# Kernel tuning notes

Measured on AMD Instinct MI355X. Metric: run time of the kernel, lower is better.

## Reference

```python
import jax, jax.numpy as jnp
import numpy as np

V, E, H, L, S, B = 32000, 1024, 512, 2, 512, 32  # vocab, emb dim, per-dir hidden, layers, seq, batch
PAD = 0
assert E == 2 * H  # required by the module's pred_emb shape assert; lets cell weights stack


def setup_inputs() -> dict:
    ks = iter(jax.random.split(jax.random.key(0), 40))
    def nrm(shape, scale=0.05):
        return jax.random.normal(next(ks), shape, dtype=jnp.float32) * scale
    seq_input = jax.random.randint(next(ks), (S, B), 1, V)
    # lengths sorted descending (pack_padded convention the torch code assumes)
    lengths = jnp.sort(jax.random.randint(next(ks), (B,), S // 2, S + 1))[::-1]
    inp = {"seq_input": seq_input, "lengths": lengths}
    for name in ("emb1", "emb2", "emb3"):
        inp[name] = nrm((V, E)).at[PAD].set(0.0)  # padding_idx row is zero
    inp["W_et"] = nrm((H, E)); inp["b_et"] = nrm((H,))      # embedding_transform
    inp["W_ct"] = nrm((H, H)); inp["b_ct"] = nrm((H,))      # context_transform
    inp["W_sc"] = nrm((1, H)); inp["b_sc"] = nrm((1,))      # to_scalar
    inp["W_g"] = nrm((E, 2 * E)); inp["b_g"] = nrm((E,))    # embedding_gate Linear
    inp["h0f"] = jax.random.uniform(next(ks), (H,), jnp.float32)  # torch.rand init params
    inp["c0f"] = jax.random.uniform(next(ks), (H,), jnp.float32)
    inp["h0b"] = jax.random.uniform(next(ks), (H,), jnp.float32)
    inp["c0b"] = jax.random.uniform(next(ks), (H,), jnp.float32)
    # LSTMCell weights: [layer, dir(fwd,bwd), 4H, in]; in==E==2H for all layers
    inp["Wih"] = nrm((L, 2, 4 * H, E))
    inp["Whh"] = nrm((L, 2, 4 * H, H))
    inp["bih"] = nrm((L, 2, 4 * H))
    inp["bhh"] = nrm((L, 2, 4 * H))
    return inp


def _lstm_cell(x, h, c, Wih, Whh, bih, bhh):
    g = x @ Wih.T + h @ Whh.T + bih + bhh
    i, f, gg, o = jnp.split(g, 4, axis=-1)
    c2 = jax.nn.sigmoid(f) * c + jax.nn.sigmoid(i) * jnp.tanh(gg)
    return jax.nn.sigmoid(o) * jnp.tanh(c2), c2


def _reverse_seq(x, lengths):
    # reverse the first `length` timesteps per batch element, keep padding in place
    t = jnp.arange(x.shape[0])[:, None]
    idx = jnp.where(t < lengths[None, :], lengths[None, :] - 1 - t, t)  # [S,B]
    idx = idx.reshape(idx.shape + (1,) * (x.ndim - 2))
    return jnp.take_along_axis(x, jnp.broadcast_to(idx, x.shape), axis=0)


def _cos(a, b):
    n = jnp.sum(a * b, -1)
    d = jnp.maximum(jnp.linalg.norm(a, axis=-1) * jnp.linalg.norm(b, axis=-1), 1e-8)
    return n / d


def _forward(seq_input, lengths, emb1, emb2, emb3, W_et, b_et, W_ct, b_ct, W_sc, b_sc,
             W_g, b_g, h0f, c0f, h0b, c0b, Wih, Whh, bih, bhh):
    Sl, Bn = seq_input.shape
    Hh = Whh.shape[-1]
    nL = Wih.shape[0]
    # active mask at step t: lengths >= t+1 (identical for forward and reversed scans)
    mask = jnp.arange(Sl)[:, None] < lengths[None, :]  # [S,B]
    h0f_b = jnp.broadcast_to(h0f, (Bn, Hh)); c0f_b = jnp.broadcast_to(c0f, (Bn, Hh))
    h0b_b = jnp.broadcast_to(h0b, (Bn, Hh)); c0b_b = jnp.broadcast_to(c0b, (Bn, Hh))
    cell = lambda l, d: (Wih[l, d], Whh[l, d], bih[l, d], bhh[l, d])

    def layer0_scan(tokens, cell_p, h0, c0):
        def step(carry, inp):
            h, c, pen = carry
            tok, m = inp
            e1, e2, e3 = emb1[tok], emb2[tok], emb3[tok]  # [B,E]
            p = (jax.nn.relu(_cos(e1, e2) - 0.3) + jax.nn.relu(_cos(e1, e3) - 0.3)
                 + jax.nn.relu(_cos(e2, e3) - 0.3))
            pen = pen + jnp.sum(jnp.where(m, p, 0.0))
            ctx = h @ W_ct.T + b_ct  # [B,H]
            sc = lambda e: jnp.tanh(e @ W_et.T + b_et + ctx) @ W_sc.T + b_sc  # [B,1]
            w = jax.nn.softmax(jnp.concatenate([sc(e1), sc(e2), sc(e3)], -1), axis=-1)
            x = w[:, :1] * e1 + w[:, 1:2] * e2 + w[:, 2:3] * e3  # attended embedding
            h2, c2 = _lstm_cell(x, h, c, *cell_p)
            mm = m[:, None]
            h = jnp.where(mm, h2, h)
            c = jnp.where(mm, c2, c)
            return (h, c, pen), (jnp.where(mm, h2, 0.0), jnp.where(mm, x, 0.0))
        (hf, cf, pen), (outs, preds) = jax.lax.scan(
            step, (h0, c0, jnp.zeros((), jnp.float32)), (tokens, mask))
        return hf, cf, outs, pen, preds

    def layer_scan(xs, cell_p, h0, c0):
        def step(carry, inp):
            h, c = carry
            x, m = inp
            h2, c2 = _lstm_cell(x, h, c, *cell_p)
            mm = m[:, None]
            return (jnp.where(mm, h2, h), jnp.where(mm, c2, c)), jnp.where(mm, h2, 0.0)
        (hf, cf), outs = jax.lax.scan(step, (h0, c0), (xs, mask))
        return hf, cf, outs

    # layer 0 with embedding attention + cosine penalty
    hF, cF, outF, penF, predF = layer0_scan(seq_input, cell(0, 0), h0f_b, c0f_b)
    hB, cB, outB, penB, predB = layer0_scan(_reverse_seq(seq_input, lengths), cell(0, 1), h0b_b, c0b_b)
    penalty = penF + penB
    predB = _reverse_seq(predB, lengths)
    gate = jax.nn.sigmoid(jnp.concatenate([predF, predB], -1) @ W_g.T + b_g)
    pred_emb = predF * gate + predB * (1.0 - gate)
    x = jnp.concatenate([outF, _reverse_seq(outB, lengths)], -1)  # [S,B,2H]
    hs = [hF, hB]; cs = [cF, cB]
    for l in range(1, nL):
        hF, cF, oF = layer_scan(x, cell(l, 0), h0f_b, c0f_b)
        hB, cB, oB = layer_scan(_reverse_seq(x, lengths), cell(l, 1), h0b_b, c0b_b)
        x = jnp.concatenate([oF, _reverse_seq(oB, lengths)], -1)
        hs += [hF, hB]; cs += [cF, cB]
    final_h = jnp.stack(hs, 0)  # [2L,B,H]
    final_c = jnp.stack(cs, 0)
    return final_h, final_c, x, penalty, pred_emb


def reference(seq_input, lengths, emb1, emb2, emb3, W_et, b_et, W_ct, b_ct, W_sc, b_sc,
              W_g, b_g, h0f, c0f, h0b, c0b, Wih, Whh, bih, bhh):
    return _forward(seq_input, lengths, emb1, emb2, emb3, W_et, b_et, W_ct, b_ct, W_sc,
                    b_sc, W_g, b_g, h0f, c0f, h0b, c0b, Wih, Whh, bih, bhh)
```

## Files before the change

### kernel.cpp

```cpp
#include <hip/hip_runtime.h>

typedef unsigned short u16;
typedef unsigned long long u64;
typedef __bf16 bf16_t;
typedef bf16_t bf16x8 __attribute__((ext_vector_type(8)));
typedef float f32x4 __attribute__((ext_vector_type(4)));

#define DEVFN static __device__ __forceinline__

constexpr int S_ = 512, B_ = 32, H_ = 512, E_ = 1024;
constexpr int SB_ = S_ * B_;

constexpr size_t OUT_FH  = 0;
constexpr size_t OUT_FC  = 65536;
constexpr size_t OUT_X   = 131072;
constexpr size_t OUT_PEN = 16908288;
constexpr size_t OUT_PE  = 16908289;

constexpr size_t WS_SLOTS = 0;
constexpr size_t WS_PEN   = 16384;
constexpr size_t WS_SPART = 16640;
constexpr size_t WS_HG0   = 41216;
constexpr size_t WS_HG1   = 106752;
constexpr size_t WS_WET   = 237824;
constexpr size_t WS_WCT   = 1286400;
constexpr size_t WS_WIH0  = 1810688;
constexpr size_t WS_WHH0  = 10199296;
constexpr size_t WS_WIH1  = 14393600;
constexpr size_t WS_WHH1  = 22782208;
constexpr size_t WS_WG    = 26976512;
constexpr size_t WS_EK    = 31170816;
constexpr size_t WS_ET    = 131834112;
constexpr size_t WS_PREDF = 232497408;
constexpr size_t WS_PREDB = 266051840;
constexpr size_t WS_OUT0F = 299606272;
constexpr size_t WS_OUT0B = 316383488;

DEVFN u16 f2bf(float f) {
  union { float f; unsigned u; } v; v.f = f;
  unsigned u = v.u;
  unsigned r = (u + 0x7fffu + ((u >> 16) & 1u)) >> 16;
  return (u16)r;
}
DEVFN float bf2f(u16 h) {
  union { unsigned u; float f; } v; v.u = ((unsigned)h) << 16;
  return v.f;
}
DEVFN float sigm(float x) { return 1.f / (1.f + __expf(-x)); }
DEVFN float tanh_f(float x) { float e = __expf(2.f * x); return 1.f - 2.f / (e + 1.f); }
DEVFN bf16x8 ld_bf8(const u16* p) { return *reinterpret_cast<const bf16x8*>(p); }
DEVFN f32x4 mfma_bf(bf16x8 a, bf16x8 b, f32x4 c) {
  return __builtin_amdgcn_mfma_f32_16x16x32_bf16(a, b, c, 0, 0, 0);
}
DEVFN void lds_st16(u16* base, int row, int rowBytes, int byteCol, bf16x8 v) {
  *reinterpret_cast<bf16x8*>((char*)base + row * rowBytes + (byteCol ^ ((row & 7) << 4))) = v;
}
DEVFN void lds_st8(u16* base, int row, int rowBytes, int byteCol, u64 v) {
  *reinterpret_cast<u64*>((char*)base + row * rowBytes + (byteCol ^ ((row & 7) << 4))) = v;
}
DEVFN bf16x8 lds_ld16(const u16* base, int row, int rowBytes, int byteCol) {
  return *reinterpret_cast<const bf16x8*>((const char*)base + row * rowBytes + (byteCol ^ ((row & 7) << 4)));
}

DEVFN u64 coh_ld64(const u64* p) {
  return __hip_atomic_load(p, __ATOMIC_RELAXED, __HIP_MEMORY_SCOPE_AGENT);
}
DEVFN void coh_st64(u64* p, u64 v) {
  __hip_atomic_store(p, v, __ATOMIC_RELAXED, __HIP_MEMORY_SCOPE_AGENT);
}
DEVFN void coh_st32(unsigned* p, unsigned v) {
  __hip_atomic_store(p, v, __ATOMIC_RELAXED, __HIP_MEMORY_SCOPE_AGENT);
}

DEVFN void gbar(unsigned* slots, int r, unsigned target) {
  __syncthreads();
  if (threadIdx.x == 0)
    __hip_atomic_store(slots + r * 16, target, __ATOMIC_RELAXED, __HIP_MEMORY_SCOPE_AGENT);
  if (threadIdx.x < 64) {
    while (__hip_atomic_load(slots + threadIdx.x * 16, __ATOMIC_RELAXED,
                             __HIP_MEMORY_SCOPE_AGENT) < target)
      __builtin_amdgcn_s_sleep(1);
  }
  __syncthreads();
}

__global__ void k_f2bf(const float* __restrict__ src, u16* __restrict__ dst, int n) {
  for (int i = blockIdx.x * blockDim.x + threadIdx.x; i < n; i += gridDim.x * blockDim.x)
    dst[i] = f2bf(src[i]);
}

__global__ __launch_bounds__(256) void k_gather(
    const int* __restrict__ seq, const int* __restrict__ lengths,
    const float* __restrict__ emb1, const float* __restrict__ emb2, const float* __restrict__ emb3,
    u16* __restrict__ eK, float* __restrict__ pen) {
  int s = blockIdx.x;
  int t = s >> 5, b = s & 31;
  int tid = threadIdx.x;
  int tok = seq[s];
  const float4* p1 = (const float4*)(emb1 + (size_t)tok * 1024);
  const float4* p2 = (const float4*)(emb2 + (size_t)tok * 1024);
  const float4* p3 = (const float4*)(emb3 + (size_t)tok * 1024);
  float4 a = p1[tid], c = p2[tid], d = p3[tid];
  size_t rb = (size_t)s * 1024 + tid * 4;
  uint2 pk;
  pk.x = f2bf(a.x) | ((unsigned)f2bf(a.y) << 16); pk.y = f2bf(a.z) | ((unsigned)f2bf(a.w) << 16);
  *(uint2*)(eK + rb) = pk;
  pk.x = f2bf(c.x) | ((unsigned)f2bf(c.y) << 16); pk.y = f2bf(c.z) | ((unsigned)f2bf(c.w) << 16);
  *(uint2*)(eK + (size_t)SB_ * 1024 + rb) = pk;
  pk.x = f2bf(d.x) | ((unsigned)f2bf(d.y) << 16); pk.y = f2bf(d.z) | ((unsigned)f2bf(d.w) << 16);
  *(uint2*)(eK + (size_t)2 * SB_ * 1024 + rb) = pk;
  float v[6];
  v[0] = a.x*c.x + a.y*c.y + a.z*c.z + a.w*c.w;
  v[1] = a.x*d.x + a.y*d.y + a.z*d.z + a.w*d.w;
  v[2] = c.x*d.x + c.y*d.y + c.z*d.z + c.w*d.w;
  v[3] = a.x*a.x + a.y*a.y + a.z*a.z + a.w*a.w;
  v[4] = c.x*c.x + c.y*c.y + c.z*c.z + c.w*c.w;
  v[5] = d.x*d.x + d.y*d.y + d.z*d.z + d.w*d.w;
  for (int i = 0; i < 6; ++i)
    for (int m = 1; m < 64; m <<= 1) v[i] += __shfl_xor(v[i], m);
  __shared__ float red[4][6];
  int wid = tid >> 6, lane = tid & 63;
  if (lane == 0) for (int i = 0; i < 6; ++i) red[wid][i] = v[i];
  __syncthreads();
  if (tid == 0) {
    float r[6];
    for (int i = 0; i < 6; ++i) r[i] = red[0][i] + red[1][i] + red[2][i] + red[3][i];
    float c12 = r[0] / fmaxf(sqrtf(r[3]) * sqrtf(r[4]), 1e-8f);
    float c13 = r[1] / fmaxf(sqrtf(r[3]) * sqrtf(r[5]), 1e-8f);
    float c23 = r[2] / fmaxf(sqrtf(r[4]) * sqrtf(r[5]), 1e-8f);
    float p = fmaxf(c12 - 0.3f, 0.f) + fmaxf(c13 - 0.3f, 0.f) + fmaxf(c23 - 0.3f, 0.f);
    if (t < lengths[b] && p > 0.f) atomicAdd(pen, 2.f * p);
  }
}

__global__ __launch_bounds__(256) void k_gemm_et(
    const u16* __restrict__ A, const u16* __restrict__ Bw,
    const float* __restrict__ bias, float* __restrict__ C) {
  int bm = blockIdx.x % 384, bn = blockIdx.x / 384;
  int m0 = bm * 128, n0 = bn * 128;
  __shared__ u16 sA[128 * 64], sB[128 * 64];
  int tid = threadIdx.x, wid = tid >> 6, lane = tid & 63;
  int wm = wid & 1, wn = wid >> 1;
  f32x4 acc[4][4] = {};
  for (int kb = 0; kb < 16; ++kb) {
    __syncthreads();
    for (int c = tid; c < 1024; c += 256) {
      int row = c >> 3, q = c & 7;
      lds_st16(sA, row, 128, q * 16, ld_bf8(A + (size_t)(m0 + row) * 1024 + kb * 64 + q * 8));
      lds_st16(sB, row, 128, q * 16, ld_bf8(Bw + (size_t)(n0 + row) * 1024 + kb * 64 + q * 8));
    }
    __syncthreads();
    for (int kk = 0; kk < 2; ++kk) {
      bf16x8 af[4], bf[4];
      int bc = kk * 64 + (lane >> 4) * 16;
      for (int i = 0; i < 4; ++i) {
        af[i] = lds_ld16(sA, wm * 64 + i * 16 + (lane & 15), 128, bc);
        bf[i] = lds_ld16(sB, wn * 64 + i * 16 + (lane & 15), 128, bc);
      }
      for (int i = 0; i < 4; ++i)
        for (int j = 0; j < 4; ++j) acc[i][j] = mfma_bf(af[i], bf[j], acc[i][j]);
    }
  }
  for (int i = 0; i < 4; ++i)
    for (int j = 0; j < 4; ++j) {
      int m = m0 + wm * 64 + i * 16 + (lane >> 4) * 4;
      int n = n0 + wn * 64 + j * 16 + (lane & 15);
      float bn_ = bias[n & 511];
      for (int r = 0; r < 4; ++r) C[(size_t)(m + r) * 512 + n] = acc[i][j][r] + bn_;
    }
}

__global__ __launch_bounds__(256) void k_gemm_gate(
    const u16* __restrict__ pF, const u16* __restrict__ pB, const u16* __restrict__ Wg,
    const float* __restrict__ bias, float* __restrict__ outPE) {
  int bm = blockIdx.x % 128, bn = blockIdx.x / 128;
  int m0 = bm * 128, n0 = bn * 128;
  __shared__ u16 sA[128 * 64], sB[128 * 64];
  int tid = threadIdx.x, wid = tid >> 6, lane = tid & 63;
  int wm = wid & 1, wn = wid >> 1;
  f32x4 acc[4][4] = {};
  for (int kb = 0; kb < 32; ++kb) {
    __syncthreads();
    const u16* Asrc = (kb < 16) ? pF : pB;
    int kof = (kb < 16) ? kb * 64 : (kb - 16) * 64;
    for (int c = tid; c < 1024; c += 256) {
      int row = c >> 3, q = c & 7;
      lds_st16(sA, row, 128, q * 16, ld_bf8(Asrc + (size_t)(m0 + row) * 1024 + kof + q * 8));
      lds_st16(sB, row, 128, q * 16, ld_bf8(Wg + (size_t)(n0 + row) * 2048 + kb * 64 + q * 8));
    }
    __syncthreads();
    for (int kk = 0; kk < 2; ++kk) {
      bf16x8 af[4], bf[4];
      int bc = kk * 64 + (lane >> 4) * 16;
      for (int i = 0; i < 4; ++i) {
        af[i] = lds_ld16(sA, wm * 64 + i * 16 + (lane & 15), 128, bc);
        bf[i] = lds_ld16(sB, wn * 64 + i * 16 + (lane & 15), 128, bc);
      }
      for (int i = 0; i < 4; ++i)
        for (int j = 0; j < 4; ++j) acc[i][j] = mfma_bf(af[i], bf[j], acc[i][j]);
    }
  }
  for (int i = 0; i < 4; ++i)
    for (int j = 0; j < 4; ++j) {
      int m = m0 + wm * 64 + i * 16 + (lane >> 4) * 4;
      int n = n0 + wn * 64 + j * 16 + (lane & 15);
      float bn_ = bias[n];
      for (int r = 0; r < 4; ++r) {
        float g = sigm(acc[i][j][r] + bn_);
        size_t idx = (size_t)(m + r) * 1024 + n;
        float a = bf2f(pF[idx]), b = bf2f(pB[idx]);
        outPE[idx] = a * g + b * (1.f - g);
      }
    }
}

__global__ __launch_bounds__(256, 1) void k_scan0(
    const u16* __restrict__ eK, const float* __restrict__ eT,
    const u16* __restrict__ wIh0, const u16* __restrict__ wHh0, const u16* __restrict__ wCt,
    const float* __restrict__ Wsc, const float* __restrict__ bct,
    const float* __restrict__ bih, const float* __restrict__ bhh,
    const int* __restrict__ lengths,
    const float* __restrict__ h0f, const float* __restrict__ c0f,
    const float* __restrict__ h0b, const float* __restrict__ c0b,
    u16* __restrict__ hg, float* __restrict__ spart,
    u16* __restrict__ out0F, u16* __restrict__ out0B,
    u16* __restrict__ predF, u16* __restrict__ predB,
    float* __restrict__ dout, unsigned* __restrict__ slots) {
  const int dir = blockIdx.x >> 6;
  const int r   = blockIdx.x & 63;
  const int tid = threadIdx.x, wid = tid >> 6, lane = tid & 63;

  const u16* Wih = wIh0 + (size_t)dir * 2048 * 1024;
  const u16* Whh = wHh0 + (size_t)dir * 2048 * 512;
  const float* bi = bih + dir * 2048;
  const float* bh = bhh + dir * 2048;
  u16* out0 = dir ? out0B : out0F;
  u16* predD = dir ? predB : predF;
  const float* h0 = dir ? h0b : h0f;
  const float* c0 = dir ? c0b : c0f;
  u16* myhg = hg + (size_t)dir * 32 * 512;
  float* spartD = spart + (size_t)dir * 3 * 32 * 32;
  unsigned* slotg = slots + dir * 64 * 16;

  __shared__ u16 sWih[32 * 1024];
  __shared__ u16 sWhh[32 * 512];
  __shared__ u16 sH[32 * 512];
  __shared__ u16 sHpub[256];
  __shared__ float sPW[3][32][32];
  __shared__ float sHW[32][32];
  __shared__ float sSK[3][32];
  __shared__ float sWt[32][4];
  __shared__ float sBias[32];

  for (int c = tid; c < 4096; c += 256) {
    int ln = c >> 7, q = c & 127;
    int n = (ln >> 3) * 512 + r * 8 + (ln & 7);
    lds_st16(sWih, ln, 2048, q * 16, ld_bf8(Wih + (size_t)n * 1024 + q * 8));
  }
  for (int c = tid; c < 2048; c += 256) {
    int ln = c >> 6, q = c & 63;
    int n = (ln >> 3) * 512 + r * 8 + (ln & 7);
    lds_st16(sWhh, ln, 1024, q * 16, ld_bf8(Whh + (size_t)n * 512 + q * 8));
  }
  if (tid < 32) {
    int n = (tid >> 3) * 512 + r * 8 + (tid & 7);
    sBias[tid] = bi[n] + bh[n];
  }

  const int pb = tid >> 3, pj = tid & 7;
  const int gj = r * 8 + pj;
  float hreg = h0[gj], creg = c0[gj];
  const int lenb = lengths[pb];

  const int Mt = wid & 1, Nt = wid >> 1;
  const int arow = Mt * 16 + (lane & 15);
  const int lenrow = lengths[arow];
  const int kq = lane >> 4;
  const int colN = Nt * 16 + (lane & 15);
  const bool isctx = (r < 32) && (wid < 2);
  int lctx[4];
  if (isctx)
    for (int reg = 0; reg < 4; ++reg) lctx[reg] = lengths[Mt * 16 + kq * 4 + reg];

  sHpub[tid] = f2bf(hreg);
  __syncthreads();
  if (tid < 64) {
    u64 v = *reinterpret_cast<const u64*>(sHpub + tid * 4);
    coh_st64((u64*)myhg + (size_t)(tid >> 1) * 128 + r * 2 + (tid & 1), v);
  }
  unsigned rnd = 0;
  gbar(slotg, r, ++rnd);

  for (int t = 0; t < 512; ++t) {
    int posA = (dir == 0) ? t : ((t < lenrow) ? (lenrow - 1 - t) : t);
    size_t ebase = (size_t)(posA * 32 + arow) * 1024;
    {
      const u64* src = (const u64*)myhg;
      u64 hv[16];
#pragma unroll
      for (int i = 0; i < 16; ++i) hv[i] = coh_ld64(src + tid + i * 256);
#pragma unroll
      for (int i = 0; i < 16; ++i) {
        int c = tid + i * 256, row = c >> 7, q = c & 127;
        lds_st8(sH, row, 1024, q * 8, hv[i]);
      }
    }
    for (int k = 0; k < 3; ++k) {
      const u16* Ek = eK + (size_t)k * SB_ * 1024 + ebase;
      f32x4 acc = {0.f, 0.f, 0.f, 0.f};
#pragma unroll 4
      for (int kb = 0; kb < 32; ++kb) {
        bf16x8 a = ld_bf8(Ek + kb * 32 + kq * 8);
        bf16x8 b = lds_ld16(sWih, colN, 2048, (kb * 32 + kq * 8) * 2);
        acc = mfma_bf(a, b, acc);
      }
      int rb = Mt * 16 + kq * 4;
      for (int reg = 0; reg < 4; ++reg) sPW[k][rb + reg][colN] = acc[reg];
    }
    __syncthreads();
    {
      f32x4 acc = {0.f, 0.f, 0.f, 0.f};
#pragma unroll 4
      for (int kb = 0; kb < 16; ++kb) {
        bf16x8 a = lds_ld16(sH, arow, 1024, (kb * 32 + kq * 8) * 2);
        bf16x8 b = lds_ld16(sWhh, colN, 1024, (kb * 32 + kq * 8) * 2);
        acc = mfma_bf(a, b, acc);
      }
      int rb = Mt * 16 + kq * 4;
      for (int reg = 0; reg < 4; ++reg) sHW[rb + reg][colN] = acc[reg];
    }
    if (isctx) {
      f32x4 acc = {0.f, 0.f, 0.f, 0.f};
      int j = r * 16 + (lane & 15);
      const u16* Wctp = wCt + (size_t)j * 512;
#pragma unroll 4
      for (int kb = 0; kb < 16; ++kb) {
        bf16x8 a = lds_ld16(sH, arow, 1024, (kb * 32 + kq * 8) * 2);
        bf16x8 b = ld_bf8(Wctp + kb * 32 + kq * 8);
        acc = mfma_bf(a, b, acc);
      }
      float wsc = Wsc[j], bctj = bct[j];
      float part[3][4];
      for (int reg = 0; reg < 4; ++reg) {
        int b = Mt * 16 + kq * 4 + reg;
        int lb = lctx[reg];
        int pos = (dir == 0) ? t : ((t < lb) ? (lb - 1 - t) : t);
        float ctx = acc[reg] + bctj;
        size_t rowoff = (size_t)(pos * 32 + b) * 512 + j;
        for (int k = 0; k < 3; ++k)
          part[k][reg] = tanh_f(eT[(size_t)k * SB_ * 512 + rowoff] + ctx) * wsc;
      }
      for (int k = 0; k < 3; ++k)
        for (int reg = 0; reg < 4; ++reg) {
          float v = part[k][reg];
          v += __shfl_xor(v, 1); v += __shfl_xor(v, 2);
          v += __shfl_xor(v, 4); v += __shfl_xor(v, 8);
          if ((lane & 15) == 0) {
            int b = Mt * 16 + kq * 4 + reg;
            union { float f; unsigned u; } w; w.f = v;
            coh_st32((unsigned*)(spartD + (k * 32 + b) * 32 + r), w.u);
          }
        }
    }
    gbar(slotg, r, ++rnd);

    if (tid < 96) {
      int k = tid >> 5, b = tid & 31;
      const u64* sp = (const u64*)(spartD + (k * 32 + b) * 32);
      float s = 0.f;
#pragma unroll
      for (int i = 0; i < 16; ++i) {
        union { u64 u; float f[2]; } w; w.u = coh_ld64(sp + i);
        s += w.f[0] + w.f[1];
      }
      sSK[k][b] = s;
    }
    __syncthreads();
    if (tid < 32) {
      float s0 = sSK[0][tid], s1 = sSK[1][tid], s2 = sSK[2][tid];
      float mx = fmaxf(s0, fmaxf(s1, s2));
      float e0 = __expf(s0 - mx), e1 = __expf(s1 - mx), e2 = __expf(s2 - mx);
      float inv = 1.f / (e0 + e1 + e2);
      sWt[tid][0] = e0 * inv; sWt[tid][1] = e1 * inv; sWt[tid][2] = e2 * inv;
    }
    __syncthreads();
    {
      float w0 = sWt[pb][0], w1 = sWt[pb][1], w2 = sWt[pb][2];
      float gq[4];
      for (int q = 0; q < 4; ++q) {
        int cl = q * 8 + pj;
        gq[q] = w0 * sPW[0][pb][cl] + w1 * sPW[1][pb][cl] + w2 * sPW[2][pb][cl]
              + sHW[pb][cl] + sBias[cl];
      }
      float ig = sigm(gq[0]), fg = sigm(gq[1]), gg = tanh_f(gq[2]), og = sigm(gq[3]);
      float c2 = fg * creg + ig * gg;
      float h2 = og * tanh_f(c2);
      bool m = (t < lenb);
      if (m) { creg = c2; hreg = h2; }
      int pos = (dir == 0) ? t : ((t < lenb) ? (lenb - 1 - t) : t);
      sHpub[tid] = f2bf(hreg);
      out0[(size_t)(pos * 32 + pb) * 512 + gj] = f2bf(m ? h2 : 0.f);
      if (t == 511) {
        dout[OUT_FH + ((size_t)dir * 32 + pb) * 512 + gj] = hreg;
        dout[OUT_FC + ((size_t)dir * 32 + pb) * 512 + gj] = creg;
      }
      size_t rowb = (size_t)(pos * 32 + pb) * 1024;
      int e0i = r * 16 + (tid & 7) * 2;
      for (int ii = 0; ii < 2; ++ii) {
        int e = e0i + ii;
        float xv = w0 * bf2f(eK[rowb + e])
                 + w1 * bf2f(eK[(size_t)SB_ * 1024 + rowb + e])
                 + w2 * bf2f(eK[(size_t)2 * SB_ * 1024 + rowb + e]);
        predD[rowb + e] = f2bf(m ? xv : 0.f);
      }
    }
    __syncthreads();
    if (tid < 64) {
      u64 v = *reinterpret_cast<const u64*>(sHpub + tid * 4);
      coh_st64((u64*)myhg + (size_t)(tid >> 1) * 128 + r * 2 + (tid & 1), v);
    }
    if (t < 511) gbar(slotg, r, ++rnd);
  }
}

__global__ __launch_bounds__(256, 1) void k_scan1(
    const u16* __restrict__ out0F, const u16* __restrict__ out0B,
    const u16* __restrict__ wIh1, const u16* __restrict__ wHh1,
    const float* __restrict__ bih, const float* __restrict__ bhh,
    const int* __restrict__ lengths,
    const float* __restrict__ h0f, const float* __restrict__ c0f,
    const float* __restrict__ h0b, const float* __restrict__ c0b,
    u16* __restrict__ hg1, float* __restrict__ dout, unsigned* __restrict__ slots) {
  const int dir = blockIdx.x >> 6;
  const int r   = blockIdx.x & 63;
  const int tid = threadIdx.x, wid = tid >> 6, lane = tid & 63;

  const u16* Wih = wIh1 + (size_t)dir * 2048 * 1024;
  const u16* Whh = wHh1 + (size_t)dir * 2048 * 512;
  const float* bi = bih + (2 + dir) * 2048;
  const float* bh = bhh + (2 + dir) * 2048;
  const float* h0 = dir ? h0b : h0f;
  const float* c0 = dir ? c0b : c0f;
  unsigned* slotg = slots + (2 + dir) * 64 * 16;

  __shared__ u16 sWih[32 * 1024];
  __shared__ u16 sWhh[32 * 512];
  __shared__ u16 sH[32 * 512];
  __shared__ u16 sHpub[256];
  __shared__ float sG[32][32];
  __shared__ float sBias[32];

  for (int c = tid; c < 4096; c += 256) {
    int ln = c >> 7, q = c & 127;
    int n = (ln >> 3) * 512 + r * 8 + (ln & 7);
    lds_st16(sWih, ln, 2048, q * 16, ld_bf8(Wih + (size_t)n * 1024 + q * 8));
  }
  for (int c = tid; c < 2048; c += 256) {
    int ln = c >> 6, q = c & 63;
    int n = (ln >> 3) * 512 + r * 8 + (ln & 7);
    lds_st16(sWhh, ln, 1024, q * 16, ld_bf8(Whh + (size_t)n * 512 + q * 8));
  }
  if (tid < 32) {
    int n = (tid >> 3) * 512 + r * 8 + (tid & 7);
    sBias[tid] = bi[n] + bh[n];
  }

  const int pb = tid >> 3, pj = tid & 7;
  const int gj = r * 8 + pj;
  float hreg = h0[gj], creg = c0[gj];
  const int lenb = lengths[pb];
  const int Mt = wid & 1, Nt = wid >> 1;
  const int arow = Mt * 16 + (lane & 15);
  const int lenrow = lengths[arow];
  const int kq = lane >> 4;
  const int colN = Nt * 16 + (lane & 15);

  sHpub[tid] = f2bf(hreg);
  __syncthreads();
  if (tid < 64) {
    u64 v = *reinterpret_cast<const u64*>(sHpub + tid * 4);
    coh_st64((u64*)(hg1 + (size_t)(0 * 2 + dir) * 32 * 512) +
             (size_t)(tid >> 1) * 128 + r * 2 + (tid & 1), v);
  }
  unsigned rnd = 0;
  gbar(slotg, r, ++rnd);

  for (int t = 0; t < 512; ++t) {
    int buf = t & 1;
    const u16* hsrc = hg1 + (size_t)(buf * 2 + dir) * 32 * 512;
    u16* hdst = hg1 + (size_t)((buf ^ 1) * 2 + dir) * 32 * 512;
    {
      const u64* src = (const u64*)hsrc;
      u64 hv[16];
#pragma unroll
      for (int i = 0; i < 16; ++i) hv[i] = coh_ld64(src + tid + i * 256);
#pragma unroll
      for (int i = 0; i < 16; ++i) {
        int c = tid + i * 256, row = c >> 7, q = c & 127;
        lds_st8(sH, row, 1024, q * 8, hv[i]);
      }
    }
    __syncthreads();
    int posA = (dir == 0) ? t : ((t < lenrow) ? (lenrow - 1 - t) : t);
    size_t rowb = (size_t)(posA * 32 + arow) * 512;
    f32x4 acc = {0.f, 0.f, 0.f, 0.f};
#pragma unroll 4
    for (int kb = 0; kb < 32; ++kb) {
      const u16* Asrc = (kb < 16) ? (out0F + rowb + kb * 32 + kq * 8)
                                  : (out0B + rowb + (kb - 16) * 32 + kq * 8);
      bf16x8 a = ld_bf8(Asrc);
      bf16x8 b = lds_ld16(sWih, colN, 2048, (kb * 32 + kq * 8) * 2);
      acc = mfma_bf(a, b, acc);
    }
#pragma unroll 4
    for (int kb = 0; kb < 16; ++kb) {
      bf16x8 a = lds_ld16(sH, arow, 1024, (kb * 32 + kq * 8) * 2);
      bf16x8 b = lds_ld16(sWhh, colN, 1024, (kb * 32 + kq * 8) * 2);
      acc = mfma_bf(a, b, acc);
    }
    {
      int rb = Mt * 16 + kq * 4;
      for (int reg = 0; reg < 4; ++reg) sG[rb + reg][colN] = acc[reg];
    }
    __syncthreads();
    {
      float gq[4];
      for (int q = 0; q < 4; ++q) gq[q] = sG[pb][q * 8 + pj] + sBias[q * 8 + pj];
      float ig = sigm(gq[0]), fg = sigm(gq[1]), gg = tanh_f(gq[2]), og = sigm(gq[3]);
      float c2 = fg * creg + ig * gg;
      float h2 = og * tanh_f(c2);
      bool m = (t < lenb);
      if (m) { creg = c2; hreg = h2; }
      int pos = (dir == 0) ? t : ((t < lenb) ? (lenb - 1 - t) : t);
      sHpub[tid] = f2bf(hreg);
      dout[OUT_X + (size_t)(pos * 32 + pb) * 1024 + dir * 512 + gj] = m ? h2 : 0.f;
      if (t == 511) {
        dout[OUT_FH + ((size_t)(2 + dir) * 32 + pb) * 512 + gj] = hreg;
        dout[OUT_FC + ((size_t)(2 + dir) * 32 + pb) * 512 + gj] = creg;
      }
    }
    __syncthreads();
    if (tid < 64) {
      u64 v = *reinterpret_cast<const u64*>(sHpub + tid * 4);
      coh_st64((u64*)hdst + (size_t)(tid >> 1) * 128 + r * 2 + (tid & 1), v);
    }
    if (t < 511) gbar(slotg, r, ++rnd);
  }
}

__global__ void k_final(const float* __restrict__ pen, float* __restrict__ dout) {
  if (threadIdx.x == 0 && blockIdx.x == 0) dout[OUT_PEN] = pen[0];
}

extern "C" void kernel_launch(void* const* d_in, const int* in_sizes, int n_in,
                              void* d_out, int out_size, void* d_ws, size_t ws_size,
                              hipStream_t stream) {
  (void)in_sizes; (void)n_in; (void)out_size; (void)ws_size;
  const int*   seq   = (const int*)d_in[0];
  const int*   lens  = (const int*)d_in[1];
  const float* emb1  = (const float*)d_in[2];
  const float* emb2  = (const float*)d_in[3];
  const float* emb3  = (const float*)d_in[4];
  const float* W_et  = (const float*)d_in[5];
  const float* b_et  = (const float*)d_in[6];
  const float* W_ct  = (const float*)d_in[7];
  const float* b_ct  = (const float*)d_in[8];
  const float* W_sc  = (const float*)d_in[9];
  const float* W_g   = (const float*)d_in[11];
  const float* b_g   = (const float*)d_in[12];
  const float* h0f   = (const float*)d_in[13];
  const float* c0f   = (const float*)d_in[14];
  const float* h0b   = (const float*)d_in[15];
  const float* c0b   = (const float*)d_in[16];
  const float* Wih   = (const float*)d_in[17];
  const float* Whh   = (const float*)d_in[18];
  const float* bih   = (const float*)d_in[19];
  const float* bhh   = (const float*)d_in[20];
  float* out = (float*)d_out;
  char* ws = (char*)d_ws;

  unsigned* slots = (unsigned*)(ws + WS_SLOTS);
  float* pen    = (float*)(ws + WS_PEN);
  float* spart  = (float*)(ws + WS_SPART);
  u16* hg0  = (u16*)(ws + WS_HG0);
  u16* hg1  = (u16*)(ws + WS_HG1);
  u16* wEt  = (u16*)(ws + WS_WET);
  u16* wCt  = (u16*)(ws + WS_WCT);
  u16* wIh0 = (u16*)(ws + WS_WIH0);
  u16* wHh0 = (u16*)(ws + WS_WHH0);
  u16* wIh1 = (u16*)(ws + WS_WIH1);
  u16* wHh1 = (u16*)(ws + WS_WHH1);
  u16* wGg  = (u16*)(ws + WS_WG);
  u16* eK   = (u16*)(ws + WS_EK);
  float* eT = (float*)(ws + WS_ET);
  u16* pF   = (u16*)(ws + WS_PREDF);
  u16* pB   = (u16*)(ws + WS_PREDB);
  u16* o0F  = (u16*)(ws + WS_OUT0F);
  u16* o0B  = (u16*)(ws + WS_OUT0B);

  hipMemsetAsync(ws, 0, 16896, stream);

  hipLaunchKernelGGL(k_f2bf, dim3(512), dim3(256), 0, stream, W_et, wEt, 524288);
  hipLaunchKernelGGL(k_f2bf, dim3(512), dim3(256), 0, stream, W_ct, wCt, 262144);
  hipLaunchKernelGGL(k_f2bf, dim3(2048), dim3(256), 0, stream, Wih, wIh0, 4194304);
  hipLaunchKernelGGL(k_f2bf, dim3(2048), dim3(256), 0, stream, Wih + 4194304, wIh1, 4194304);
  hipLaunchKernelGGL(k_f2bf, dim3(1024), dim3(256), 0, stream, Whh, wHh0, 2097152);
  hipLaunchKernelGGL(k_f2bf, dim3(1024), dim3(256), 0, stream, Whh + 2097152, wHh1, 2097152);
  hipLaunchKernelGGL(k_f2bf, dim3(1024), dim3(256), 0, stream, W_g, wGg, 2097152);

  hipLaunchKernelGGL(k_gather, dim3(SB_), dim3(256), 0, stream,
                     seq, lens, emb1, emb2, emb3, eK, pen);
  hipLaunchKernelGGL(k_gemm_et, dim3(1536), dim3(256), 0, stream, eK, wEt, b_et, eT);
  hipLaunchKernelGGL(k_scan0, dim3(128), dim3(256), 0, stream,
                     eK, eT, wIh0, wHh0, wCt, W_sc, b_ct, bih, bhh, lens,
                     h0f, c0f, h0b, c0b, hg0, spart, o0F, o0B, pF, pB, out, slots);
  hipLaunchKernelGGL(k_scan1, dim3(128), dim3(256), 0, stream,
                     o0F, o0B, wIh1, wHh1, bih, bhh, lens,
                     h0f, c0f, h0b, c0b, hg1, out, slots);
  hipLaunchKernelGGL(k_gemm_gate, dim3(1024), dim3(256), 0, stream,
                     pF, pB, wGg, b_g, out + OUT_PE);
  hipLaunchKernelGGL(k_final, dim3(1), dim3(64), 0, stream, pen, out);
}
```

Measured before the change: 16.36 ms.

## Split grid barrier into arrive/wait and overlap input projections with barrier latency

The grid barrier is split into separate arrive and wait phases. In both recurrent layer kernels, the input-to-hidden MFMA work, which does not depend on the recurrent state, now runs between arrive and wait: in layer 0 inside the attention barrier, and in layer 1 it is computed for the next timestep while waiting. Output stores are also placed after the arrive. The time loop now stops at the maximum sequence length (lengths[0]) instead of 512, and the padded tail rows are zero-filled afterwards. This relies on lengths being sorted in descending order and adds register pressure for the carried accumulator.

Result: faster. 14.44 ms (-11.7%).

```diff
diff --git a/kernel.cpp b/kernel.cpp
--- a/kernel.cpp
+++ b/kernel.cpp
@@ -72,16 +72,22 @@
   __hip_atomic_store(p, v, __ATOMIC_RELAXED, __HIP_MEMORY_SCOPE_AGENT);
 }
 
-DEVFN void gbar(unsigned* slots, int r, unsigned target) {
+DEVFN void gbar_arrive(unsigned* slots, int r, unsigned target) {
   __syncthreads();
   if (threadIdx.x == 0)
     __hip_atomic_store(slots + r * 16, target, __ATOMIC_RELAXED, __HIP_MEMORY_SCOPE_AGENT);
+}
+DEVFN void gbar_wait(unsigned* slots, unsigned target) {
   if (threadIdx.x < 64) {
     while (__hip_atomic_load(slots + threadIdx.x * 16, __ATOMIC_RELAXED,
                              __HIP_MEMORY_SCOPE_AGENT) < target)
       __builtin_amdgcn_s_sleep(1);
   }
   __syncthreads();
+}
+DEVFN void gbar(unsigned* slots, int r, unsigned target) {
+  gbar_arrive(slots, r, target);
+  gbar_wait(slots, target);
 }
 
 __global__ void k_f2bf(const float* __restrict__ src, u16* __restrict__ dst, int n) {
@@ -271,6 +277,7 @@
   const int gj = r * 8 + pj;
   float hreg = h0[gj], creg = c0[gj];
   const int lenb = lengths[pb];
+  const int Lmax = lengths[0];
 
   const int Mt = wid & 1, Nt = wid >> 1;
   const int arow = Mt * 16 + (lane & 15);
@@ -291,9 +298,8 @@
   unsigned rnd = 0;
   gbar(slotg, r, ++rnd);
 
-  for (int t = 0; t < 512; ++t) {
-    int posA = (dir == 0) ? t : ((t < lenrow) ? (lenrow - 1 - t) : t);
-    size_t ebase = (size_t)(posA * 32 + arow) * 1024;
+  for (int t = 0; t < Lmax; ++t) {
+    const bool last = (t == Lmax - 1);
     {
       const u64* src = (const u64*)myhg;
       u64 hv[16];
@@ -304,18 +310,6 @@
         int c = tid + i * 256, row = c >> 7, q = c & 127;
         lds_st8(sH, row, 1024, q * 8, hv[i]);
       }
-    }
-    for (int k = 0; k < 3; ++k) {
-      const u16* Ek = eK + (size_t)k * SB_ * 1024 + ebase;
-      f32x4 acc = {0.f, 0.f, 0.f, 0.f};
-#pragma unroll 4
-      for (int kb = 0; kb < 32; ++kb) {
-        bf16x8 a = ld_bf8(Ek + kb * 32 + kq * 8);
-        bf16x8 b = lds_ld16(sWih, colN, 2048, (kb * 32 + kq * 8) * 2);
-        acc = mfma_bf(a, b, acc);
-      }
-      int rb = Mt * 16 + kq * 4;
-      for (int reg = 0; reg < 4; ++reg) sPW[k][rb + reg][colN] = acc[reg];
     }
     __syncthreads();
     {
@@ -362,7 +356,25 @@
           }
         }
     }
-    gbar(slotg, r, ++rnd);
+    unsigned rndA = ++rnd;
+    gbar_arrive(slotg, r, rndA);
+    {
+      int posA = (dir == 0) ? t : ((t < lenrow) ? (lenrow - 1 - t) : t);
+      size_t ebase = (size_t)(posA * 32 + arow) * 1024;
+      for (int k = 0; k < 3; ++k) {
+        const u16* Ek = eK + (size_t)k * SB_ * 1024 + ebase;
+        f32x4 acc = {0.f, 0.f, 0.f, 0.f};
+#pragma unroll 4
+        for (int kb = 0; kb < 32; ++kb) {
+          bf16x8 a = ld_bf8(Ek + kb * 32 + kq * 8);
+          bf16x8 b = lds_ld16(sWih, colN, 2048, (kb * 32 + kq * 8) * 2);
+          acc = mfma_bf(a, b, acc);
+        }
+        int rb = Mt * 16 + kq * 4;
+        for (int reg = 0; reg < 4; ++reg) sPW[k][rb + reg][colN] = acc[reg];
+      }
+    }
+    gbar_wait(slotg, rndA);
 
     if (tid < 96) {
       int k = tid >> 5, b = tid & 31;
@@ -384,8 +396,9 @@
       sWt[tid][0] = e0 * inv; sWt[tid][1] = e1 * inv; sWt[tid][2] = e2 * inv;
     }
     __syncthreads();
-    {
-      float w0 = sWt[pb][0], w1 = sWt[pb][1], w2 = sWt[pb][2];
+    float w0 = sWt[pb][0], w1 = sWt[pb][1], w2 = sWt[pb][2];
+    float h2, c2; bool m; int pos;
+    {
       float gq[4];
       for (int q = 0; q < 4; ++q) {
         int cl = q * 8 + pj;
@@ -393,17 +406,25 @@
               + sHW[pb][cl] + sBias[cl];
       }
       float ig = sigm(gq[0]), fg = sigm(gq[1]), gg = tanh_f(gq[2]), og = sigm(gq[3]);
-      float c2 = fg * creg + ig * gg;
-      float h2 = og * tanh_f(c2);
-      bool m = (t < lenb);
+      c2 = fg * creg + ig * gg;
+      h2 = og * tanh_f(c2);
+      m = (t < lenb);
       if (m) { creg = c2; hreg = h2; }
-      int pos = (dir == 0) ? t : ((t < lenb) ? (lenb - 1 - t) : t);
+      pos = (dir == 0) ? t : ((t < lenb) ? (lenb - 1 - t) : t);
       sHpub[tid] = f2bf(hreg);
+    }
+    unsigned rndB = 0;
+    if (!last) {
+      __syncthreads();
+      if (tid < 64) {
+        u64 v = *reinterpret_cast<const u64*>(sHpub + tid * 4);
+        coh_st64((u64*)myhg + (size_t)(tid >> 1) * 128 + r * 2 + (tid & 1), v);
+      }
+      rndB = ++rnd;
+      gbar_arrive(slotg, r, rndB);
+    }
+    {
       out0[(size_t)(pos * 32 + pb) * 512 + gj] = f2bf(m ? h2 : 0.f);
-      if (t == 511) {
-        dout[OUT_FH + ((size_t)dir * 32 + pb) * 512 + gj] = hreg;
-        dout[OUT_FC + ((size_t)dir * 32 + pb) * 512 + gj] = creg;
-      }
       size_t rowb = (size_t)(pos * 32 + pb) * 1024;
       int e0i = r * 16 + (tid & 7) * 2;
       for (int ii = 0; ii < 2; ++ii) {
@@ -414,12 +435,14 @@
         predD[rowb + e] = f2bf(m ? xv : 0.f);
       }
     }
-    __syncthreads();
-    if (tid < 64) {
-      u64 v = *reinterpret_cast<const u64*>(sHpub + tid * 4);
-      coh_st64((u64*)myhg + (size_t)(tid >> 1) * 128 + r * 2 + (tid & 1), v);
-    }
-    if (t < 511) gbar(slotg, r, ++rnd);
+    if (!last) gbar_wait(slotg, rndB);
+  }
+
+  dout[OUT_FH + ((size_t)dir * 32 + pb) * 512 + gj] = hreg;
+  dout[OUT_FC + ((size_t)dir * 32 + pb) * 512 + gj] = creg;
+  for (int row = Lmax * 32 + r; row < SB_; row += 64) {
+    if (tid < 128) ((u64*)(out0 + (size_t)row * 512))[tid] = 0;
+    ((u64*)(predD + (size_t)row * 1024))[tid] = 0;
   }
 }
 
@@ -469,11 +492,25 @@
   const int gj = r * 8 + pj;
   float hreg = h0[gj], creg = c0[gj];
   const int lenb = lengths[pb];
+  const int Lmax = lengths[0];
   const int Mt = wid & 1, Nt = wid >> 1;
   const int arow = Mt * 16 + (lane & 15);
   const int lenrow = lengths[arow];
   const int kq = lane >> 4;
   const int colN = Nt * 16 + (lane & 15);
+
+  __syncthreads();
+  f32x4 accx = {0.f, 0.f, 0.f, 0.f};
+  {
+    int posA = (dir == 0) ? 0 : (lenrow - 1);
+    size_t rowb = (size_t)(posA * 32 + arow) * 512;
+#pragma unroll 4
+    for (int kb = 0; kb < 32; ++kb) {
+      const u16* Asrc = (kb < 16) ? (out0F + rowb + kb * 32 + kq * 8)
+                                  : (out0B + rowb + (kb - 16) * 32 + kq * 8);
+      accx = mfma_bf(ld_bf8(Asrc), lds_ld16(sWih, colN, 2048, (kb * 32 + kq * 8) * 2), accx);
+    }
+  }
 
   sHpub[tid] = f2bf(hreg);
   __syncthreads();
@@ -485,7 +522,8 @@
   unsigned rnd = 0;
   gbar(slotg, r, ++rnd);
 
-  for (int t = 0; t < 512; ++t) {
+  for (int t = 0; t < Lmax; ++t) {
+    const bool last = (t == Lmax - 1);
     int buf = t & 1;
     const u16* hsrc = hg1 + (size_t)(buf * 2 + dir) * 32 * 512;
     u16* hdst = hg1 + (size_t)((buf ^ 1) * 2 + dir) * 32 * 512;
@@ -501,17 +539,7 @@
       }
     }
     __syncthreads();
-    int posA = (dir == 0) ? t : ((t < lenrow) ? (lenrow - 1 - t) : t);
-    size_t rowb = (size_t)(posA * 32 + arow) * 512;
-    f32x4 acc = {0.f, 0.f, 0.f, 0.f};
-#pragma unroll 4
-    for (int kb = 0; kb < 32; ++kb) {
-      const u16* Asrc = (kb < 16) ? (out0F + rowb + kb * 32 + kq * 8)
-                                  : (out0B + rowb + (kb - 16) * 32 + kq * 8);
-      bf16x8 a = ld_bf8(Asrc);
-      bf16x8 b = lds_ld16(sWih, colN, 2048, (kb * 32 + kq * 8) * 2);
-      acc = mfma_bf(a, b, acc);
-    }
+    f32x4 acc = accx;
 #pragma unroll 4
     for (int kb = 0; kb < 16; ++kb) {
       bf16x8 a = lds_ld16(sH, arow, 1024, (kb * 32 + kq * 8) * 2);
@@ -523,28 +551,49 @@
       for (int reg = 0; reg < 4; ++reg) sG[rb + reg][colN] = acc[reg];
     }
     __syncthreads();
+    float h2, c2; bool m; int pos;
     {
       float gq[4];
       for (int q = 0; q < 4; ++q) gq[q] = sG[pb][q * 8 + pj] + sBias[q * 8 + pj];
       float ig = sigm(gq[0]), fg = sigm(gq[1]), gg = tanh_f(gq[2]), og = sigm(gq[3]);
-      float c2 = fg * creg + ig * gg;
-      float h2 = og * tanh_f(c2);
-      bool m = (t < lenb);
+      c2 = fg * creg + ig * gg;
+      h2 = og * tanh_f(c2);
+      m = (t < lenb);
       if (m) { creg = c2; hreg = h2; }
-      int pos = (dir == 0) ? t : ((t < lenb) ? (lenb - 1 - t) : t);
+      pos = (dir == 0) ? t : ((t < lenb) ? (lenb - 1 - t) : t);
       sHpub[tid] = f2bf(hreg);
-      dout[OUT_X + (size_t)(pos * 32 + pb) * 1024 + dir * 512 + gj] = m ? h2 : 0.f;
-      if (t == 511) {
-        dout[OUT_FH + ((size_t)(2 + dir) * 32 + pb) * 512 + gj] = hreg;
-        dout[OUT_FC + ((size_t)(2 + dir) * 32 + pb) * 512 + gj] = creg;
-      }
-    }
-    __syncthreads();
-    if (tid < 64) {
-      u64 v = *reinterpret_cast<const u64*>(sHpub + tid * 4);
-      coh_st64((u64*)hdst + (size_t)(tid >> 1) * 128 + r * 2 + (tid & 1), v);
-    }
-    if (t < 511) gbar(slotg, r, ++rnd);
+    }
+    unsigned rndB = 0;
+    if (!last) {
+      __syncthreads();
+      if (tid < 64) {
+        u64 v = *reinterpret_cast<const u64*>(sHpub + tid * 4);
+        coh_st64((u64*)hdst + (size_t)(tid >> 1) * 128 + r * 2 + (tid & 1), v);
+      }
+      rndB = ++rnd;
+      gbar_arrive(slotg, r, rndB);
+    }
+    dout[OUT_X + (size_t)(pos * 32 + pb) * 1024 + dir * 512 + gj] = m ? h2 : 0.f;
+    if (!last) {
+      int tn = t + 1;
+      int posA = (dir == 0) ? tn : ((tn < lenrow) ? (lenrow - 1 - tn) : tn);
+      size_t rowb = (size_t)(posA * 32 + arow) * 512;
+      f32x4 ax = {0.f, 0.f, 0.f, 0.f};
+#pragma unroll 4
+      for (int kb = 0; kb < 32; ++kb) {
+        const u16* Asrc = (kb < 16) ? (out0F + rowb + kb * 32 + kq * 8)
+                                    : (out0B + rowb + (kb - 16) * 32 + kq * 8);
+        ax = mfma_bf(ld_bf8(Asrc), lds_ld16(sWih, colN, 2048, (kb * 32 + kq * 8) * 2), ax);
+      }
+      accx = ax;
+      gbar_wait(slotg, rndB);
+    }
+  }
+
+  dout[OUT_FH + ((size_t)(2 + dir) * 32 + pb) * 512 + gj] = hreg;
+  dout[OUT_FC + ((size_t)(2 + dir) * 32 + pb) * 512 + gj] = creg;
+  for (int row = Lmax * 32 + r; row < SB_; row += 64) {
+    ((u64*)(dout + OUT_X + (size_t)row * 1024 + dir * 512))[tid] = 0;
   }
 }
 
```
